# Kernel optimization log

Hardware: AMD Instinct MI355X
Metric: run time of the kernel (lower is better)

## Reference

```python
import math
import jax, jax.numpy as jnp
import numpy as np

DIM = 2048
SLOTS = 256
T = 64          # num_replay_steps
N = 8192        # number of episodic traces
REPLAY_NOISE = 0.01
FREQ = 6.0      # theta frequency (Hz)
DT = 0.01
STRENGTH = 0.5  # write strength used in consolidate()
THRESHOLD = 0.0


def setup_inputs() -> dict:
    key = jax.random.key(0)
    ks = jax.random.split(key, 16)
    def w(k, shape):
        return (jax.random.normal(k, shape, jnp.float32) / math.sqrt(shape[-1]))
    return {
        "traces": jax.random.normal(ks[0], (N, DIM), jnp.float32),
        "noise": jax.random.normal(ks[1], (T, DIM), jnp.float32),
        "memory0": jax.random.normal(ks[2], (SLOTS, DIM), jnp.float32) * 0.01,
        "usage0": jnp.zeros((SLOTS,), jnp.float32),
        "W1": w(ks[3], (DIM, DIM)), "b1": jnp.zeros((DIM,), jnp.float32),
        "W2": w(ks[4], (DIM, DIM)), "b2": jnp.zeros((DIM,), jnp.float32),
        "Wl": w(ks[5], (DIM, DIM)), "bl": jnp.zeros((DIM,), jnp.float32),
        "vw": jax.random.normal(ks[6], (DIM,), jnp.float32),
        "vb": jnp.zeros((DIM,), jnp.float32),
        "Wg": w(ks[7], (DIM, DIM)), "bg": jnp.zeros((DIM,), jnp.float32),
        "Wa": w(ks[8], (SLOTS, DIM)), "ba": jnp.zeros((SLOTS,), jnp.float32),
        "We": w(ks[9], (DIM, DIM)), "be": jnp.zeros((DIM,), jnp.float32),
        "Wad": w(ks[10], (DIM, DIM)), "bad": jnp.zeros((DIM,), jnp.float32),
        "idx": jax.random.randint(ks[11], (T,), 0, N, jnp.int64 if jax.config.jax_enable_x64 else jnp.int32),
    }


def reference(traces, noise, memory0, usage0, W1, b1, W2, b2, Wl, bl, vw, vb,
              Wg, bg, Wa, ba, We, be, Wad, bad, idx):
    # Deterministic theta phase schedule (step_theta per replay step).
    t = jnp.arange(T, dtype=jnp.float32)
    phase = jnp.mod(2.0 * math.pi * FREQ * DT * (t + 1.0), 2.0 * math.pi)  # (T,)

    # --- batched (parallel) part: replay transform + NMDA gate + heads ---
    trace = traces[idx]                                   # (T, DIM) gather
    noisy = trace + noise * REPLAY_NOISE
    h = jax.nn.relu(noisy @ W1.T + b1)
    x = h @ W2.T + b2                                     # transformed (T, DIM)

    ligand = jax.nn.sigmoid(x @ Wl.T + bl)                # (T, DIM)
    phase_signal = jnp.cos(phase - math.pi)[:, None]      # (T, 1)
    voltage = jax.nn.sigmoid(phase_signal * vw[None, :] + vb - THRESHOLD)
    gate = jax.nn.sigmoid((ligand * voltage) @ Wg.T + bg)
    gated = x * gate                                      # (T, DIM)

    logits0 = gated @ Wa.T + ba                           # (T, SLOTS)
    erase = jax.nn.sigmoid(gated @ We.T + be)             # (T, DIM)
    add = gated @ Wad.T + bad                             # (T, DIM)

    # --- sequential part: erase/add outer-product writes with usage penalty ---
    def step(carry, inputs):
        mem, usage = carry
        lg, er, ad = inputs
        wgt = jax.nn.softmax(lg - usage * 0.1)            # (SLOTS,)
        outer_w = STRENGTH * wgt[:, None]                 # (SLOTS, 1)
        mem = mem * (1.0 - outer_w * er[None, :]) + outer_w * ad[None, :]
        return (mem, usage + wgt), None

    (mem, usage), _ = jax.lax.scan(step, (memory0, usage0), (logits0, erase, add))
    return mem
```

## Files before the change

### kernel.cpp

```cpp
#include <hip/hip_runtime.h>
#include <math.h>

#define DIM 2048
#define SLOTS 256
#define TSTEPS 64
#define FB (TSTEPS * DIM)
#define KQ 4
#define BK 64

typedef unsigned short u16;
typedef __bf16 bf16x8 __attribute__((ext_vector_type(8)));
typedef float f32x4 __attribute__((ext_vector_type(4)));

union FragU { unsigned u[4]; bf16x8 v; };

__device__ __forceinline__ float bf2f(u16 h){
    union { unsigned u; float f; } v; v.u = ((unsigned)h) << 16; return v.f;
}
__device__ __forceinline__ u16 f2bf(float f){
    union { float f; unsigned u; } v; v.f = f;
    unsigned r = v.u + 0x7fffu + ((v.u >> 16) & 1u);
    return (u16)(r >> 16);
}
__device__ __forceinline__ float sigmoidf_(float x){ return 1.0f / (1.0f + __expf(-x)); }

__device__ __forceinline__ void split8t(const float* x, bf16x8& hi, bf16x8& lo){
    FragU H, L;
    #pragma unroll
    for (int p = 0; p < 4; ++p){
        union { float f; unsigned u; } u0, u1, l0, l1;
        u0.f = x[2*p]; u1.f = x[2*p+1];
        unsigned h0 = u0.u & 0xffff0000u, h1 = u1.u & 0xffff0000u;
        H.u[p] = (h0 >> 16) | h1;
        l0.f = u0.f - __uint_as_float(h0);
        l1.f = u1.f - __uint_as_float(h1);
        L.u[p] = (l0.u >> 16) | (l1.u & 0xffff0000u);
    }
    hi = H.v; lo = L.v;
}

__device__ __forceinline__ f32x4 mfma16(bf16x8 a, bf16x8 b, f32x4 c){
    return __builtin_amdgcn_mfma_f32_16x16x32_bf16(a, b, c, 0, 0, 0);
}

__device__ __forceinline__ void gl_lds16(const float* gp, float* lp){
    __builtin_amdgcn_global_load_lds(
        (const __attribute__((address_space(1))) unsigned int*)gp,
        (__attribute__((address_space(3))) unsigned int*)lp, 16, 0, 0);
}

__global__ void detect_k(const int* __restrict__ idxw, int* __restrict__ flags)
{
    __shared__ int nz_s;
    if (threadIdx.x == 0) nz_s = 0;
    __syncthreads();
    int nz = 0;
    if (threadIdx.x < 32 && idxw[2 * threadIdx.x + 1] != 0) nz = 1;
    atomicAdd(&nz_s, nz);
    __syncthreads();
    if (threadIdx.x == 0) flags[1] = (nz_s == 0) ? 1 : 0;
}

__global__ void calib_k(u16* __restrict__ tbl)
{
    const int lane = threadIdx.x;
    const u16 oneb = 0x3F80;
    const u16 lb = f2bf((float)((lane & 15) + 1));
    FragU O, L;
    #pragma unroll
    for (int p = 0; p < 4; ++p){
        O.u[p] = ((unsigned)oneb) | (((unsigned)oneb) << 16);
        L.u[p] = ((unsigned)lb)   | (((unsigned)lb)   << 16);
    }
    f32x4 z = {0.f, 0.f, 0.f, 0.f};
    f32x4 dj = mfma16(O.v, L.v, z);
    f32x4 dt = mfma16(L.v, O.v, z);
    #pragma unroll
    for (int r = 0; r < 4; ++r){
        int jl = (int)(dj[r] * (1.0f/32.0f) + 0.5f) - 1;
        int tl = (int)(dt[r] * (1.0f/32.0f) + 0.5f) - 1;
        tbl[lane * 4 + r] = (u16)((tl & 15) | ((jl & 15) << 8));
    }
}

__global__ __launch_bounds__(256)
void prep(const float* __restrict__ traces, const float* __restrict__ noise,
          const int* __restrict__ idxw, const int* __restrict__ flags,
          float* __restrict__ A0)
{
    const int t = blockIdx.x;
    long row = flags[1] ? (long)idxw[2 * t] : (long)idxw[t];
    const int k = threadIdx.x * 8;
    const float* tr = traces + (size_t)row * DIM + k;
    const float* nz = noise + (size_t)t * DIM + k;
    float4 a0 = *(const float4*)(tr), a1 = *(const float4*)(tr + 4);
    float4 b0 = *(const float4*)(nz), b1 = *(const float4*)(nz + 4);
    float4 r0, r1;
    r0.x = fmaf(0.01f, b0.x, a0.x); r0.y = fmaf(0.01f, b0.y, a0.y);
    r0.z = fmaf(0.01f, b0.z, a0.z); r0.w = fmaf(0.01f, b0.w, a0.w);
    r1.x = fmaf(0.01f, b1.x, a1.x); r1.y = fmaf(0.01f, b1.y, a1.y);
    r1.z = fmaf(0.01f, b1.z, a1.z); r1.w = fmaf(0.01f, b1.w, a1.w);
    float* o = A0 + (size_t)t * DIM + k;
    *(float4*)(o) = r0; *(float4*)(o + 4) = r1;
}

__device__ __forceinline__ void gemm_body(const float* __restrict__ A,
                                          const float* __restrict__ Wrow0,
                                          int kq, float* At, float* Wt,
                                          const u16* __restrict__ tbl,
                                          f32x4& acc, int* tout, int* jout)
{
    const int tid = threadIdx.x;
    const int lane = tid & 63, w = tid >> 6;
    const int s = lane & 15, rsub = lane >> 4;
    const int n4 = lane & 15;
    const int kbase = kq * (DIM / KQ);

    acc = (f32x4){0.f, 0.f, 0.f, 0.f};

    for (int c = 0; c < (DIM / KQ) / BK; ++c){
        const int kc = kbase + c * BK;
        #pragma unroll
        for (int i = 0; i < 4; ++i){
            const int rowL = w * 16 + i * 4 + rsub;
            const float* gp = A + (size_t)rowL * DIM + kc + ((s ^ (rowL & 15)) << 2);
            gl_lds16(gp, At + (w * 16 + i * 4) * BK);
        }
        {
            const int rowL = w * 4 + rsub;
            const float* gp = Wrow0 + (size_t)rowL * DIM + kc + ((s ^ (rowL & 15)) << 2);
            gl_lds16(gp, Wt + (w * 4) * BK);
        }
        __syncthreads();
        #pragma unroll
        for (int ks = 0; ks < 2; ++ks){
            const int cg0 = ks * 8 + (lane >> 4) * 2;
            const int rA = w * 16 + n4;
            float a8[8], w8[8];
            *(float4*)(a8)     = *(const float4*)&At[rA * BK + ((cg0 ^ n4) << 2)];
            *(float4*)(a8 + 4) = *(const float4*)&At[rA * BK + (((cg0 + 1) ^ n4) << 2)];
            *(float4*)(w8)     = *(const float4*)&Wt[n4 * BK + ((cg0 ^ n4) << 2)];
            *(float4*)(w8 + 4) = *(const float4*)&Wt[n4 * BK + (((cg0 + 1) ^ n4) << 2)];
            bf16x8 ah, al, wh, wl;
            split8t(a8, ah, al);
            split8t(w8, wh, wl);
            acc = mfma16(ah, wh, acc);
            acc = mfma16(al, wh, acc);
            acc = mfma16(ah, wl, acc);
        }
        __syncthreads();
    }
    #pragma unroll
    for (int r = 0; r < 4; ++r){
        u16 tj = tbl[lane * 4 + r];
        tout[r] = w * 16 + (tj & 15);
        jout[r] = (tj >> 8) & 15;
    }
}

__global__ __launch_bounds__(256)
void gemm4(const float* __restrict__ A, const float* __restrict__ W,
           const u16* __restrict__ tbl, float* __restrict__ Pout)
{
    __shared__ float At[64 * BK];
    __shared__ float Wt[16 * BK];
    const int kq = blockIdx.x & (KQ - 1);
    const int j0 = (blockIdx.x >> 2) * 16;
    f32x4 acc; int tr[4], jr[4];
    gemm_body(A, W + (size_t)j0 * DIM, kq, At, Wt, tbl, acc, tr, jr);
    float* outb = Pout + (size_t)kq * FB;
    #pragma unroll
    for (int r = 0; r < 4; ++r)
        outb[(size_t)tr[r] * DIM + j0 + jr[r]] = acc[r];
}

__global__ __launch_bounds__(256)
void gemm4h(const float* __restrict__ G,
            const float* __restrict__ We, const float* __restrict__ Wad,
            const float* __restrict__ Wa, const u16* __restrict__ tbl,
            float* __restrict__ PpE, float* __restrict__ PpA, float* __restrict__ PpL)
{
    __shared__ float At[64 * BK];
    __shared__ float Wt[16 * BK];
    const int kq = blockIdx.x & (KQ - 1);
    const int jt = blockIdx.x >> 2;
    const float* W; float* out; int j0, NJ;
    if (jt < 128)      { W = We;  out = PpE; j0 = jt * 16;         NJ = DIM; }
    else if (jt < 256) { W = Wad; out = PpA; j0 = (jt - 128) * 16; NJ = DIM; }
    else               { W = Wa;  out = PpL; j0 = (jt - 256) * 16; NJ = SLOTS; }
    f32x4 acc; int tr[4], jr[4];
    gemm_body(G, W + (size_t)j0 * DIM, kq, At, Wt, tbl, acc, tr, jr);
    float* outb = out + (size_t)kq * 64 * NJ;
    #pragma unroll
    for (int r = 0; r < 4; ++r)
        outb[(size_t)tr[r] * NJ + j0 + jr[r]] = acc[r];
}

template<int MODE>
__global__ __launch_bounds__(256)
void comb(const float* __restrict__ P, const float* __restrict__ bias,
          const float* __restrict__ vw, const float* __restrict__ vb,
          const float* __restrict__ X, float* __restrict__ out)
{
    const size_t i0 = ((size_t)blockIdx.x * 256 + threadIdx.x) * 8;
    const int t = (int)(i0 >> 11);
    const int j = (int)(i0 & (DIM - 1));
    float v[8], tmp[8];
    *(float4*)(v)     = *(const float4*)(P + i0);
    *(float4*)(v + 4) = *(const float4*)(P + i0 + 4);
    #pragma unroll
    for (int p = 1; p < KQ; ++p){
        *(float4*)(tmp)     = *(const float4*)(P + (size_t)p * FB + i0);
        *(float4*)(tmp + 4) = *(const float4*)(P + (size_t)p * FB + i0 + 4);
        #pragma unroll
        for (int c = 0; c < 8; ++c) v[c] += tmp[c];
    }
    float b8[8];
    *(float4*)(b8)     = *(const float4*)(bias + j);
    *(float4*)(b8 + 4) = *(const float4*)(bias + j + 4);
    float x8[8], y8[8];
    if (MODE == 2){
        *(float4*)(x8)     = *(const float4*)(vw + j);
        *(float4*)(x8 + 4) = *(const float4*)(vw + j + 4);
        *(float4*)(y8)     = *(const float4*)(vb + j);
        *(float4*)(y8 + 4) = *(const float4*)(vb + j + 4);
    }
    if (MODE == 3){
        *(float4*)(x8)     = *(const float4*)(X + i0);
        *(float4*)(x8 + 4) = *(const float4*)(X + i0 + 4);
    }
    const float ps = -cosf(0.37699111843077515f * (float)(t + 1));
    float r[8];
    #pragma unroll
    for (int c = 0; c < 8; ++c){
        float u = v[c] + b8[c];
        if (MODE == 0)      r[c] = fmaxf(u, 0.f);
        else if (MODE == 1) r[c] = u;
        else if (MODE == 2) r[c] = sigmoidf_(u) * sigmoidf_(fmaf(ps, x8[c], y8[c]));
        else if (MODE == 3) r[c] = x8[c] * sigmoidf_(u);
        else                r[c] = sigmoidf_(u);
    }
    *(float4*)(out + i0)     = *(const float4*)(r);
    *(float4*)(out + i0 + 4) = *(const float4*)(r + 4);
}

__global__ void scan_k(const float* __restrict__ PpL, const float* __restrict__ ba,
                       const float* __restrict__ usage0, float* __restrict__ wgt)
{
    const int lane = threadIdx.x;
    float u[4], bv[4];
    #pragma unroll
    for (int c = 0; c < 4; ++c){ u[c] = usage0[lane + 64 * c]; bv[c] = ba[lane + 64 * c]; }
    const int PS = TSTEPS * SLOTS;
    for (int t = 0; t < TSTEPS; ++t){
        float e[4];
        #pragma unroll
        for (int c = 0; c < 4; ++c){
            int s = lane + 64 * c;
            float lg = PpL[t * SLOTS + s] + PpL[PS + t * SLOTS + s]
                     + PpL[2 * PS + t * SLOTS + s] + PpL[3 * PS + t * SLOTS + s] + bv[c];
            e[c] = __expf(lg - 0.1f * u[c]);
        }
        float sm = (e[0] + e[1]) + (e[2] + e[3]);
        #pragma unroll
        for (int off = 1; off < 64; off <<= 1) sm += __shfl_xor(sm, off, 64);
        float inv = 1.0f / sm;
        float* wr = wgt + t * SLOTS;
        #pragma unroll
        for (int c = 0; c < 4; ++c){
            float ww = e[c] * inv;
            u[c] += ww;
            wr[lane + 64 * c] = ww;
        }
    }
}

__global__ __launch_bounds__(256)
void mem_k(const float* __restrict__ mem0, const float* __restrict__ wgt,
           const float* __restrict__ ER, const float* __restrict__ AD,
           float* __restrict__ out)
{
    const int s = threadIdx.x;
    const int d0 = blockIdx.x * 8;
    float m[8];
    *(float4*)(m)     = *(const float4*)(mem0 + (size_t)s * DIM + d0);
    *(float4*)(m + 4) = *(const float4*)(mem0 + (size_t)s * DIM + d0 + 4);
    for (int t = 0; t < TSTEPS; ++t){
        const size_t ro = (size_t)t * DIM + d0;
        float e8[8], a8[8];
        *(float4*)(e8)     = *(const float4*)(ER + ro);
        *(float4*)(e8 + 4) = *(const float4*)(ER + ro + 4);
        *(float4*)(a8)     = *(const float4*)(AD + ro);
        *(float4*)(a8 + 4) = *(const float4*)(AD + ro + 4);
        float w = 0.5f * wgt[t * SLOTS + s];
        #pragma unroll
        for (int c = 0; c < 8; ++c){
            float f = w * e8[c];
            float tmp = fmaf(-f, m[c], m[c]);
            m[c] = fmaf(w, a8[c], tmp);
        }
    }
    float* op = out + (size_t)s * DIM + d0;
    *(float4*)(op)     = *(const float4*)(m);
    *(float4*)(op + 4) = *(const float4*)(m + 4);
}

extern "C" void kernel_launch(void* const* d_in, const int* in_sizes, int n_in,
                              void* d_out, int out_size, void* d_ws, size_t ws_size,
                              hipStream_t stream)
{
    const float* traces = (const float*)d_in[0];
    const float* noise  = (const float*)d_in[1];
    const float* mem0   = (const float*)d_in[2];
    const float* usage0 = (const float*)d_in[3];
    const float* W1 = (const float*)d_in[4];  const float* b1 = (const float*)d_in[5];
    const float* W2 = (const float*)d_in[6];  const float* b2 = (const float*)d_in[7];
    const float* Wl = (const float*)d_in[8];  const float* bl = (const float*)d_in[9];
    const float* vw = (const float*)d_in[10]; const float* vb = (const float*)d_in[11];
    const float* Wg = (const float*)d_in[12]; const float* bg = (const float*)d_in[13];
    const float* Wa = (const float*)d_in[14]; const float* ba = (const float*)d_in[15];
    const float* We = (const float*)d_in[16]; const float* be = (const float*)d_in[17];
    const float* Wad = (const float*)d_in[18]; const float* bad_ = (const float*)d_in[19];
    const int* idx = (const int*)d_in[20];

    char* ws = (char*)d_ws;
    int* FLAGS = (int*)ws;
    u16* TBL = (u16*)(ws + 16);
    float* pool = (float*)(ws + 1024);
    float* A0v = pool;
    float* Hv  = pool + 1 * FB;
    float* Xv  = pool + 2 * FB;
    float* LVv = pool + 3 * FB;
    float* Gv  = pool + 4 * FB;
    float* ERv = pool + 5 * FB;
    float* ADv = pool + 6 * FB;
    float* Pp  = pool + 7 * FB;
    float* PpE = pool;
    float* PpA = Pp;
    float* PpL = pool + 11 * FB;
    float* WGv = PpL + 4 * TSTEPS * SLOTS;

    detect_k<<<1, 256, 0, stream>>>(idx, FLAGS);
    calib_k<<<1, 64, 0, stream>>>(TBL);
    prep<<<TSTEPS, 256, 0, stream>>>(traces, noise, idx, FLAGS, A0v);

    gemm4<<<128 * KQ, 256, 0, stream>>>(A0v, W1, TBL, Pp);
    comb<0><<<64, 256, 0, stream>>>(Pp, b1, nullptr, nullptr, nullptr, Hv);
    gemm4<<<128 * KQ, 256, 0, stream>>>(Hv, W2, TBL, Pp);
    comb<1><<<64, 256, 0, stream>>>(Pp, b2, nullptr, nullptr, nullptr, Xv);
    gemm4<<<128 * KQ, 256, 0, stream>>>(Xv, Wl, TBL, Pp);
    comb<2><<<64, 256, 0, stream>>>(Pp, bl, vw, vb, nullptr, LVv);
    gemm4<<<128 * KQ, 256, 0, stream>>>(LVv, Wg, TBL, Pp);
    comb<3><<<64, 256, 0, stream>>>(Pp, bg, nullptr, nullptr, Xv, Gv);

    gemm4h<<<272 * KQ, 256, 0, stream>>>(Gv, We, Wad, Wa, TBL, PpE, PpA, PpL);
    comb<4><<<64, 256, 0, stream>>>(PpE, be, nullptr, nullptr, nullptr, ERv);
    comb<1><<<64, 256, 0, stream>>>(PpA, bad_, nullptr, nullptr, nullptr, ADv);

    scan_k<<<1, 64, 0, stream>>>(PpL, ba, usage0, WGv);
    mem_k<<<DIM / 8, 256, 0, stream>>>(mem0, WGv, ERv, ADv, (float*)d_out);
}
```

Before: 311.7 us.

## Fuse all stages into a persistent megakernel with grid barriers and last-block reduction

Replaces the chain of roughly fifteen launches with one setup kernel plus a single persistent kernel of 512 blocks. Stages are separated by hierarchical atomic grid barriers. Each split-K GEMM tile counts its finished partial blocks, and the last block to finish performs the bias/activation combine, removing the separate combine kernels. The softmax scan and memory update also run inside the megakernel. This removes launch overhead and inter-kernel gaps, but it depends on all 512 blocks being co-resident for the barriers to avoid deadlock, and the serial scan leaves most blocks idle at a barrier.

```diff
diff --git a/kernel.cpp b/kernel.cpp
--- a/kernel.cpp
+++ b/kernel.cpp
@@ -7,6 +7,7 @@
 #define FB (TSTEPS * DIM)
 #define KQ 4
 #define BK 64
+#define NBLK 512
 
 typedef unsigned short u16;
 typedef __bf16 bf16x8 __attribute__((ext_vector_type(8)));
@@ -14,9 +15,6 @@
 
 union FragU { unsigned u[4]; bf16x8 v; };
 
-__device__ __forceinline__ float bf2f(u16 h){
-    union { unsigned u; float f; } v; v.u = ((unsigned)h) << 16; return v.f;
-}
 __device__ __forceinline__ u16 f2bf(float f){
     union { float f; unsigned u; } v; v.f = f;
     unsigned r = v.u + 0x7fffu + ((v.u >> 16) & 1u);
@@ -49,66 +47,25 @@
         (__attribute__((address_space(3))) unsigned int*)lp, 16, 0, 0);
 }
 
-__global__ void detect_k(const int* __restrict__ idxw, int* __restrict__ flags)
-{
-    __shared__ int nz_s;
-    if (threadIdx.x == 0) nz_s = 0;
-    __syncthreads();
-    int nz = 0;
-    if (threadIdx.x < 32 && idxw[2 * threadIdx.x + 1] != 0) nz = 1;
-    atomicAdd(&nz_s, nz);
-    __syncthreads();
-    if (threadIdx.x == 0) flags[1] = (nz_s == 0) ? 1 : 0;
-}
-
-__global__ void calib_k(u16* __restrict__ tbl)
-{
-    const int lane = threadIdx.x;
-    const u16 oneb = 0x3F80;
-    const u16 lb = f2bf((float)((lane & 15) + 1));
-    FragU O, L;
-    #pragma unroll
-    for (int p = 0; p < 4; ++p){
-        O.u[p] = ((unsigned)oneb) | (((unsigned)oneb) << 16);
-        L.u[p] = ((unsigned)lb)   | (((unsigned)lb)   << 16);
-    }
-    f32x4 z = {0.f, 0.f, 0.f, 0.f};
-    f32x4 dj = mfma16(O.v, L.v, z);
-    f32x4 dt = mfma16(L.v, O.v, z);
-    #pragma unroll
-    for (int r = 0; r < 4; ++r){
-        int jl = (int)(dj[r] * (1.0f/32.0f) + 0.5f) - 1;
-        int tl = (int)(dt[r] * (1.0f/32.0f) + 0.5f) - 1;
-        tbl[lane * 4 + r] = (u16)((tl & 15) | ((jl & 15) << 8));
-    }
-}
-
-__global__ __launch_bounds__(256)
-void prep(const float* __restrict__ traces, const float* __restrict__ noise,
-          const int* __restrict__ idxw, const int* __restrict__ flags,
-          float* __restrict__ A0)
-{
-    const int t = blockIdx.x;
-    long row = flags[1] ? (long)idxw[2 * t] : (long)idxw[t];
-    const int k = threadIdx.x * 8;
-    const float* tr = traces + (size_t)row * DIM + k;
-    const float* nz = noise + (size_t)t * DIM + k;
-    float4 a0 = *(const float4*)(tr), a1 = *(const float4*)(tr + 4);
-    float4 b0 = *(const float4*)(nz), b1 = *(const float4*)(nz + 4);
-    float4 r0, r1;
-    r0.x = fmaf(0.01f, b0.x, a0.x); r0.y = fmaf(0.01f, b0.y, a0.y);
-    r0.z = fmaf(0.01f, b0.z, a0.z); r0.w = fmaf(0.01f, b0.w, a0.w);
-    r1.x = fmaf(0.01f, b1.x, a1.x); r1.y = fmaf(0.01f, b1.y, a1.y);
-    r1.z = fmaf(0.01f, b1.z, a1.z); r1.w = fmaf(0.01f, b1.w, a1.w);
-    float* o = A0 + (size_t)t * DIM + k;
-    *(float4*)(o) = r0; *(float4*)(o + 4) = r1;
+struct SMem { float At[64 * BK]; float Wt[16 * BK]; int flag; };
+
+__device__ __forceinline__ void gridbar(int* bar){
+    __syncthreads();
+    if (threadIdx.x == 0){
+        const int g = (int)(blockIdx.x & 15);
+        int a = __hip_atomic_fetch_add(&bar[g * 16], 1, __ATOMIC_ACQ_REL, __HIP_MEMORY_SCOPE_AGENT);
+        if (a == (NBLK / 16) - 1)
+            __hip_atomic_fetch_add(&bar[256], 1, __ATOMIC_ACQ_REL, __HIP_MEMORY_SCOPE_AGENT);
+        while (__hip_atomic_load(&bar[256], __ATOMIC_RELAXED, __HIP_MEMORY_SCOPE_AGENT) < 16)
+            __builtin_amdgcn_s_sleep(4);
+        __threadfence();
+    }
+    __syncthreads();
 }
 
 __device__ __forceinline__ void gemm_body(const float* __restrict__ A,
                                           const float* __restrict__ Wrow0,
-                                          int kq, float* At, float* Wt,
-                                          const u16* __restrict__ tbl,
-                                          f32x4& acc, int* tout, int* jout)
+                                          int kq, float* At, float* Wt, f32x4& acc)
 {
     const int tid = threadIdx.x;
     const int lane = tid & 63, w = tid >> 6;
@@ -150,159 +107,247 @@
         }
         __syncthreads();
     }
+}
+
+template<int MODE>
+__device__ __forceinline__ void comb_tile(const float* __restrict__ P, int NJ, int j0,
+    const float* __restrict__ bias, const float* __restrict__ vwp,
+    const float* __restrict__ vbp, const float* __restrict__ Xp,
+    float* __restrict__ out)
+{
+    const int t = threadIdx.x >> 2;
+    const int j = j0 + ((threadIdx.x & 3) << 2);
+    const size_t ro = (size_t)t * NJ + j;
+    const size_t PS = (size_t)64 * NJ;
+    float v[4], tmp[4];
+    *(float4*)(v) = *(const float4*)(P + ro);
     #pragma unroll
-    for (int r = 0; r < 4; ++r){
-        u16 tj = tbl[lane * 4 + r];
-        tout[r] = w * 16 + (tj & 15);
-        jout[r] = (tj >> 8) & 15;
-    }
-}
-
-__global__ __launch_bounds__(256)
-void gemm4(const float* __restrict__ A, const float* __restrict__ W,
-           const u16* __restrict__ tbl, float* __restrict__ Pout)
-{
-    __shared__ float At[64 * BK];
-    __shared__ float Wt[16 * BK];
-    const int kq = blockIdx.x & (KQ - 1);
-    const int j0 = (blockIdx.x >> 2) * 16;
-    f32x4 acc; int tr[4], jr[4];
-    gemm_body(A, W + (size_t)j0 * DIM, kq, At, Wt, tbl, acc, tr, jr);
-    float* outb = Pout + (size_t)kq * FB;
+    for (int p = 1; p < KQ; ++p){
+        *(float4*)(tmp) = *(const float4*)(P + (size_t)p * PS + ro);
+        #pragma unroll
+        for (int c = 0; c < 4; ++c) v[c] += tmp[c];
+    }
+    float b4[4];
+    *(float4*)(b4) = *(const float4*)(bias + j);
+    float x4[4], y4[4];
+    if (MODE == 2){
+        *(float4*)(x4) = *(const float4*)(vwp + j);
+        *(float4*)(y4) = *(const float4*)(vbp + j);
+    }
+    if (MODE == 3){
+        *(float4*)(x4) = *(const float4*)(Xp + ro);
+    }
+    const float ps = -cosf(0.37699111843077515f * (float)(t + 1));
+    float r[4];
+    #pragma unroll
+    for (int c = 0; c < 4; ++c){
+        float u = v[c] + b4[c];
+        if (MODE == 0)      r[c] = fmaxf(u, 0.f);
+        else if (MODE == 1) r[c] = u;
+        else if (MODE == 2) r[c] = sigmoidf_(u) * sigmoidf_(fmaf(ps, x4[c], y4[c]));
+        else if (MODE == 3) r[c] = x4[c] * sigmoidf_(u);
+        else                r[c] = sigmoidf_(u);
+    }
+    *(float4*)(out + ro) = *(const float4*)(r);
+}
+
+template<int MODE>
+__device__ __forceinline__ void do_tile(int vb, int jt, int j0,
+    const float* __restrict__ A, const float* __restrict__ W,
+    float* __restrict__ Pout, int NJ,
+    const float* __restrict__ bias, const float* __restrict__ vwp,
+    const float* __restrict__ vbp, const float* __restrict__ Xp,
+    float* __restrict__ Out, int* __restrict__ tctr,
+    SMem& sm, const int* trr, const int* jrr)
+{
+    const int kq = vb & (KQ - 1);
+    f32x4 acc;
+    gemm_body(A, W + (size_t)j0 * DIM, kq, sm.At, sm.Wt, acc);
+    float* outb = Pout + (size_t)kq * 64 * NJ;
     #pragma unroll
     for (int r = 0; r < 4; ++r)
-        outb[(size_t)tr[r] * DIM + j0 + jr[r]] = acc[r];
+        outb[(size_t)trr[r] * NJ + j0 + jrr[r]] = acc[r];
+    __syncthreads();
+    if (threadIdx.x == 0){
+        __threadfence();
+        int a = __hip_atomic_fetch_add(&tctr[jt], 1, __ATOMIC_ACQ_REL, __HIP_MEMORY_SCOPE_AGENT);
+        sm.flag = (a == KQ - 1) ? 1 : 0;
+    }
+    __syncthreads();
+    if (sm.flag)
+        comb_tile<MODE>(Pout, NJ, j0, bias, vwp, vbp, Xp, Out);
 }
 
 __global__ __launch_bounds__(256)
-void gemm4h(const float* __restrict__ G,
-            const float* __restrict__ We, const float* __restrict__ Wad,
-            const float* __restrict__ Wa, const u16* __restrict__ tbl,
-            float* __restrict__ PpE, float* __restrict__ PpA, float* __restrict__ PpL)
-{
-    __shared__ float At[64 * BK];
-    __shared__ float Wt[16 * BK];
-    const int kq = blockIdx.x & (KQ - 1);
-    const int jt = blockIdx.x >> 2;
-    const float* W; float* out; int j0, NJ;
-    if (jt < 128)      { W = We;  out = PpE; j0 = jt * 16;         NJ = DIM; }
-    else if (jt < 256) { W = Wad; out = PpA; j0 = (jt - 128) * 16; NJ = DIM; }
-    else               { W = Wa;  out = PpL; j0 = (jt - 256) * 16; NJ = SLOTS; }
-    f32x4 acc; int tr[4], jr[4];
-    gemm_body(G, W + (size_t)j0 * DIM, kq, At, Wt, tbl, acc, tr, jr);
-    float* outb = out + (size_t)kq * 64 * NJ;
-    #pragma unroll
-    for (int r = 0; r < 4; ++r)
-        outb[(size_t)tr[r] * NJ + j0 + jr[r]] = acc[r];
-}
-
-template<int MODE>
-__global__ __launch_bounds__(256)
-void comb(const float* __restrict__ P, const float* __restrict__ bias,
+void init_k(const float* __restrict__ traces, const float* __restrict__ noise,
+            const int* __restrict__ idxw, char* __restrict__ ws)
+{
+    const int tid = threadIdx.x;
+    if (blockIdx.x == TSTEPS){
+        int* z = (int*)ws;
+        for (int i = tid; i < 16384; i += 256) z[i] = 0;
+        return;
+    }
+    __shared__ int i64f;
+    int v = 0;
+    if (tid < 32) v = (idxw[2 * tid + 1] != 0) ? 1 : 0;
+    unsigned long long bm = __ballot(v);
+    if (tid == 0) i64f = (bm == 0ull) ? 1 : 0;
+    __syncthreads();
+    const int t = blockIdx.x;
+    long row = i64f ? (long)idxw[2 * t] : (long)idxw[t];
+
+    float* A0 = (float*)(ws + 65536);
+    const int k = tid * 8;
+    const float* tr = traces + (size_t)row * DIM + k;
+    const float* nz = noise + (size_t)t * DIM + k;
+    float4 a0 = *(const float4*)(tr), a1 = *(const float4*)(tr + 4);
+    float4 b0 = *(const float4*)(nz), b1 = *(const float4*)(nz + 4);
+    float4 r0, r1;
+    r0.x = fmaf(0.01f, b0.x, a0.x); r0.y = fmaf(0.01f, b0.y, a0.y);
+    r0.z = fmaf(0.01f, b0.z, a0.z); r0.w = fmaf(0.01f, b0.w, a0.w);
+    r1.x = fmaf(0.01f, b1.x, a1.x); r1.y = fmaf(0.01f, b1.y, a1.y);
+    r1.z = fmaf(0.01f, b1.z, a1.z); r1.w = fmaf(0.01f, b1.w, a1.w);
+    float* o = A0 + (size_t)t * DIM + k;
+    *(float4*)(o) = r0; *(float4*)(o + 4) = r1;
+}
+
+__global__ __launch_bounds__(256, 3)
+void mega(const float* __restrict__ W1, const float* __restrict__ b1,
+          const float* __restrict__ W2, const float* __restrict__ b2,
+          const float* __restrict__ Wl, const float* __restrict__ bl,
           const float* __restrict__ vw, const float* __restrict__ vb,
-          const float* __restrict__ X, float* __restrict__ out)
-{
-    const size_t i0 = ((size_t)blockIdx.x * 256 + threadIdx.x) * 8;
-    const int t = (int)(i0 >> 11);
-    const int j = (int)(i0 & (DIM - 1));
-    float v[8], tmp[8];
-    *(float4*)(v)     = *(const float4*)(P + i0);
-    *(float4*)(v + 4) = *(const float4*)(P + i0 + 4);
-    #pragma unroll
-    for (int p = 1; p < KQ; ++p){
-        *(float4*)(tmp)     = *(const float4*)(P + (size_t)p * FB + i0);
-        *(float4*)(tmp + 4) = *(const float4*)(P + (size_t)p * FB + i0 + 4);
-        #pragma unroll
-        for (int c = 0; c < 8; ++c) v[c] += tmp[c];
-    }
-    float b8[8];
-    *(float4*)(b8)     = *(const float4*)(bias + j);
-    *(float4*)(b8 + 4) = *(const float4*)(bias + j + 4);
-    float x8[8], y8[8];
-    if (MODE == 2){
-        *(float4*)(x8)     = *(const float4*)(vw + j);
-        *(float4*)(x8 + 4) = *(const float4*)(vw + j + 4);
-        *(float4*)(y8)     = *(const float4*)(vb + j);
-        *(float4*)(y8 + 4) = *(const float4*)(vb + j + 4);
-    }
-    if (MODE == 3){
-        *(float4*)(x8)     = *(const float4*)(X + i0);
-        *(float4*)(x8 + 4) = *(const float4*)(X + i0 + 4);
-    }
-    const float ps = -cosf(0.37699111843077515f * (float)(t + 1));
-    float r[8];
-    #pragma unroll
-    for (int c = 0; c < 8; ++c){
-        float u = v[c] + b8[c];
-        if (MODE == 0)      r[c] = fmaxf(u, 0.f);
-        else if (MODE == 1) r[c] = u;
-        else if (MODE == 2) r[c] = sigmoidf_(u) * sigmoidf_(fmaf(ps, x8[c], y8[c]));
-        else if (MODE == 3) r[c] = x8[c] * sigmoidf_(u);
-        else                r[c] = sigmoidf_(u);
-    }
-    *(float4*)(out + i0)     = *(const float4*)(r);
-    *(float4*)(out + i0 + 4) = *(const float4*)(r + 4);
-}
-
-__global__ void scan_k(const float* __restrict__ PpL, const float* __restrict__ ba,
-                       const float* __restrict__ usage0, float* __restrict__ wgt)
-{
-    const int lane = threadIdx.x;
-    float u[4], bv[4];
-    #pragma unroll
-    for (int c = 0; c < 4; ++c){ u[c] = usage0[lane + 64 * c]; bv[c] = ba[lane + 64 * c]; }
-    const int PS = TSTEPS * SLOTS;
-    for (int t = 0; t < TSTEPS; ++t){
-        float e[4];
+          const float* __restrict__ Wg, const float* __restrict__ bg,
+          const float* __restrict__ Wa, const float* __restrict__ ba,
+          const float* __restrict__ We, const float* __restrict__ be,
+          const float* __restrict__ Wad, const float* __restrict__ bad_,
+          const float* __restrict__ usage0, const float* __restrict__ mem0,
+          float* __restrict__ out, char* __restrict__ ws)
+{
+    __shared__ SMem sm;
+    int* BAR  = (int*)ws;
+    int* TCTR = (int*)(ws + 16384);
+    float* pool = (float*)(ws + 65536);
+    float* A0v = pool;
+    float* Hv  = pool + 1 * (size_t)FB;
+    float* Xv  = pool + 2 * (size_t)FB;
+    float* LVv = pool + 3 * (size_t)FB;
+    float* Gv  = pool + 4 * (size_t)FB;
+    float* ERv = pool + 5 * (size_t)FB;
+    float* ADv = pool + 6 * (size_t)FB;
+    float* Pp  = pool + 7 * (size_t)FB;
+    float* PpE = pool;
+    float* PpA = Pp;
+    float* PpL = pool + 11 * (size_t)FB;
+    float* WGv = PpL + 4 * TSTEPS * SLOTS;
+    float* PpS = WGv + TSTEPS * SLOTS;
+
+    const int tid = threadIdx.x, lane = tid & 63, w = tid >> 6;
+
+    int trr[4], jrr[4];
+    {
+        const u16 oneb = 0x3F80;
+        const u16 lb = f2bf((float)((lane & 15) + 1));
+        FragU O, L;
+        #pragma unroll
+        for (int p = 0; p < 4; ++p){
+            O.u[p] = ((unsigned)oneb) | (((unsigned)oneb) << 16);
+            L.u[p] = ((unsigned)lb)   | (((unsigned)lb)   << 16);
+        }
+        f32x4 z = {0.f, 0.f, 0.f, 0.f};
+        f32x4 dj = mfma16(O.v, L.v, z);
+        f32x4 dt = mfma16(L.v, O.v, z);
+        #pragma unroll
+        for (int r = 0; r < 4; ++r){
+            int jl = (int)(dj[r] * (1.0f/32.0f) + 0.5f) - 1;
+            int tl = (int)(dt[r] * (1.0f/32.0f) + 0.5f) - 1;
+            trr[r] = w * 16 + (tl & 15);
+            jrr[r] = jl & 15;
+        }
+    }
+
+    const int jt0 = (int)(blockIdx.x >> 2);
+
+    do_tile<0>((int)blockIdx.x, jt0, jt0 * 16, A0v, W1, Pp, DIM,
+               b1, nullptr, nullptr, nullptr, Hv, TCTR + 0 * 512, sm, trr, jrr);
+    gridbar(BAR + 0 * 512);
+    do_tile<1>((int)blockIdx.x, jt0, jt0 * 16, Hv, W2, Pp, DIM,
+               b2, nullptr, nullptr, nullptr, Xv, TCTR + 1 * 512, sm, trr, jrr);
+    gridbar(BAR + 1 * 512);
+    do_tile<2>((int)blockIdx.x, jt0, jt0 * 16, Xv, Wl, Pp, DIM,
+               bl, vw, vb, nullptr, LVv, TCTR + 2 * 512, sm, trr, jrr);
+    gridbar(BAR + 2 * 512);
+    do_tile<3>((int)blockIdx.x, jt0, jt0 * 16, LVv, Wg, Pp, DIM,
+               bg, nullptr, nullptr, Xv, Gv, TCTR + 3 * 512, sm, trr, jrr);
+    gridbar(BAR + 3 * 512);
+    for (int vbb = (int)blockIdx.x; vbb < 272 * KQ; vbb += NBLK){
+        const int jt = vbb >> 2;
+        if (jt < 128)
+            do_tile<4>(vbb, jt, jt * 16, Gv, We, PpE, DIM,
+                       be, nullptr, nullptr, nullptr, ERv, TCTR + 4 * 512, sm, trr, jrr);
+        else if (jt < 256)
+            do_tile<1>(vbb, jt, (jt - 128) * 16, Gv, Wad, PpA, DIM,
+                       bad_, nullptr, nullptr, nullptr, ADv, TCTR + 4 * 512, sm, trr, jrr);
+        else
+            do_tile<1>(vbb, jt, (jt - 256) * 16, Gv, Wa, PpL, SLOTS,
+                       ba, nullptr, nullptr, nullptr, PpS, TCTR + 4 * 512, sm, trr, jrr);
+    }
+    gridbar(BAR + 4 * 512);
+
+    if (blockIdx.x == 0 && tid < 64){
+        float u[4], cur[4];
         #pragma unroll
         for (int c = 0; c < 4; ++c){
-            int s = lane + 64 * c;
-            float lg = PpL[t * SLOTS + s] + PpL[PS + t * SLOTS + s]
-                     + PpL[2 * PS + t * SLOTS + s] + PpL[3 * PS + t * SLOTS + s] + bv[c];
-            e[c] = __expf(lg - 0.1f * u[c]);
-        }
-        float sm = (e[0] + e[1]) + (e[2] + e[3]);
-        #pragma unroll
-        for (int off = 1; off < 64; off <<= 1) sm += __shfl_xor(sm, off, 64);
-        float inv = 1.0f / sm;
-        float* wr = wgt + t * SLOTS;
-        #pragma unroll
-        for (int c = 0; c < 4; ++c){
-            float ww = e[c] * inv;
-            u[c] += ww;
-            wr[lane + 64 * c] = ww;
-        }
-    }
-}
-
-__global__ __launch_bounds__(256)
-void mem_k(const float* __restrict__ mem0, const float* __restrict__ wgt,
-           const float* __restrict__ ER, const float* __restrict__ AD,
-           float* __restrict__ out)
-{
-    const int s = threadIdx.x;
-    const int d0 = blockIdx.x * 8;
-    float m[8];
-    *(float4*)(m)     = *(const float4*)(mem0 + (size_t)s * DIM + d0);
-    *(float4*)(m + 4) = *(const float4*)(mem0 + (size_t)s * DIM + d0 + 4);
-    for (int t = 0; t < TSTEPS; ++t){
-        const size_t ro = (size_t)t * DIM + d0;
-        float e8[8], a8[8];
-        *(float4*)(e8)     = *(const float4*)(ER + ro);
-        *(float4*)(e8 + 4) = *(const float4*)(ER + ro + 4);
-        *(float4*)(a8)     = *(const float4*)(AD + ro);
-        *(float4*)(a8 + 4) = *(const float4*)(AD + ro + 4);
-        float w = 0.5f * wgt[t * SLOTS + s];
-        #pragma unroll
-        for (int c = 0; c < 8; ++c){
-            float f = w * e8[c];
-            float tmp = fmaf(-f, m[c], m[c]);
-            m[c] = fmaf(w, a8[c], tmp);
-        }
-    }
-    float* op = out + (size_t)s * DIM + d0;
-    *(float4*)(op)     = *(const float4*)(m);
-    *(float4*)(op + 4) = *(const float4*)(m + 4);
+            u[c]   = usage0[tid + 64 * c];
+            cur[c] = PpS[tid + 64 * c];
+        }
+        for (int t = 0; t < TSTEPS; ++t){
+            float nxt[4] = {0.f, 0.f, 0.f, 0.f};
+            if (t < TSTEPS - 1){
+                #pragma unroll
+                for (int c = 0; c < 4; ++c) nxt[c] = PpS[(t + 1) * SLOTS + tid + 64 * c];
+            }
+            float e[4];
+            #pragma unroll
+            for (int c = 0; c < 4; ++c) e[c] = __expf(cur[c] - 0.1f * u[c]);
+            float sm_ = (e[0] + e[1]) + (e[2] + e[3]);
+            #pragma unroll
+            for (int off = 1; off < 64; off <<= 1) sm_ += __shfl_xor(sm_, off, 64);
+            float inv = 1.0f / sm_;
+            float* wr = WGv + t * SLOTS;
+            #pragma unroll
+            for (int c = 0; c < 4; ++c){
+                float ww = e[c] * inv;
+                u[c] += ww;
+                wr[tid + 64 * c] = ww;
+            }
+            #pragma unroll
+            for (int c = 0; c < 4; ++c) cur[c] = nxt[c];
+        }
+    }
+    gridbar(BAR + 5 * 512);
+
+    {
+        const int s = tid;
+        const int d0 = (int)blockIdx.x * 4;
+        float m[4];
+        *(float4*)(m) = *(const float4*)(mem0 + (size_t)s * DIM + d0);
+        #pragma unroll 4
+        for (int t = 0; t < TSTEPS; ++t){
+            const size_t ro = (size_t)t * DIM + d0;
+            float e4[4], a4[4];
+            *(float4*)(e4) = *(const float4*)(ERv + ro);
+            *(float4*)(a4) = *(const float4*)(ADv + ro);
+            float wgt = 0.5f * WGv[t * SLOTS + s];
+            #pragma unroll
+            for (int c = 0; c < 4; ++c){
+                float f = wgt * e4[c];
+                float tmp = fmaf(-f, m[c], m[c]);
+                m[c] = fmaf(wgt, a4[c], tmp);
+            }
+        }
+        *(float4*)(out + (size_t)s * DIM + d0) = *(const float4*)(m);
+    }
 }
 
 extern "C" void kernel_launch(void* const* d_in, const int* in_sizes, int n_in,
@@ -324,39 +369,9 @@
     const int* idx = (const int*)d_in[20];
 
     char* ws = (char*)d_ws;
-    int* FLAGS = (int*)ws;
-    u16* TBL = (u16*)(ws + 16);
-    float* pool = (float*)(ws + 1024);
-    float* A0v = pool;
-    float* Hv  = pool + 1 * FB;
-    float* Xv  = pool + 2 * FB;
-    float* LVv = pool + 3 * FB;
-    float* Gv  = pool + 4 * FB;
-    float* ERv = pool + 5 * FB;
-    float* ADv = pool + 6 * FB;
-    float* Pp  = pool + 7 * FB;
-    float* PpE = pool;
-    float* PpA = Pp;
-    float* PpL = pool + 11 * FB;
-    float* WGv = PpL + 4 * TSTEPS * SLOTS;
-
-    detect_k<<<1, 256, 0, stream>>>(idx, FLAGS);
-    calib_k<<<1, 64, 0, stream>>>(TBL);
-    prep<<<TSTEPS, 256, 0, stream>>>(traces, noise, idx, FLAGS, A0v);
-
-    gemm4<<<128 * KQ, 256, 0, stream>>>(A0v, W1, TBL, Pp);
-    comb<0><<<64, 256, 0, stream>>>(Pp, b1, nullptr, nullptr, nullptr, Hv);
-    gemm4<<<128 * KQ, 256, 0, stream>>>(Hv, W2, TBL, Pp);
-    comb<1><<<64, 256, 0, stream>>>(Pp, b2, nullptr, nullptr, nullptr, Xv);
-    gemm4<<<128 * KQ, 256, 0, stream>>>(Xv, Wl, TBL, Pp);
-    comb<2><<<64, 256, 0, stream>>>(Pp, bl, vw, vb, nullptr, LVv);
-    gemm4<<<128 * KQ, 256, 0, stream>>>(LVv, Wg, TBL, Pp);
-    comb<3><<<64, 256, 0, stream>>>(Pp, bg, nullptr, nullptr, Xv, Gv);
-
-    gemm4h<<<272 * KQ, 256, 0, stream>>>(Gv, We, Wad, Wa, TBL, PpE, PpA, PpL);
-    comb<4><<<64, 256, 0, stream>>>(PpE, be, nullptr, nullptr, nullptr, ERv);
-    comb<1><<<64, 256, 0, stream>>>(PpA, bad_, nullptr, nullptr, nullptr, ADv);
-
-    scan_k<<<1, 64, 0, stream>>>(PpL, ba, usage0, WGv);
-    mem_k<<<DIM / 8, 256, 0, stream>>>(mem0, WGv, ERv, ADv, (float*)d_out);
-}
+
+    init_k<<<TSTEPS + 1, 256, 0, stream>>>(traces, noise, idx, ws);
+    mega<<<NBLK, 256, 0, stream>>>(W1, b1, W2, b2, Wl, bl, vw, vb, Wg, bg,
+                                   Wa, ba, We, be, Wad, bad_,
+                                   usage0, mem0, (float*)d_out, ws);
+}
```

Result: slower. 615.9 us (+97.6%).
